# Kernel tuning notes

Hardware: AMD Instinct MI355X
Metric: run time of the kernel (lower is better)

## Reference

```python
import jax, jax.numpy as jnp
import numpy as np
import math

DMODEL, DK, H, DFF = 1024, 64, 16, 4096
B, T = 2, 2048
EPS = 1e-5


def setup_inputs() -> dict:
    key = jax.random.key(0)
    ks = jax.random.split(key, 12)
    s = 0.02
    x = jax.random.normal(ks[0], (B, T, DMODEL), dtype=jnp.float32)
    # causal mask, broadcastable [1,1,T,T]; 0 -> masked (like masked_fill(mask==0, -inf))
    attention_mask = jnp.tril(jnp.ones((T, T), dtype=jnp.int32))[None, None]
    Wq = jax.random.normal(ks[1], (DMODEL, DK * H), dtype=jnp.float32) * s
    bq = jnp.zeros((DK * H,), jnp.float32)
    Wk = jax.random.normal(ks[2], (DMODEL, DK * H), dtype=jnp.float32) * s
    bk = jnp.zeros((DK * H,), jnp.float32)
    Wv = jax.random.normal(ks[3], (DMODEL, DMODEL), dtype=jnp.float32) * s
    bv = jnp.zeros((DMODEL,), jnp.float32)
    W1 = jax.random.normal(ks[4], (DMODEL, DFF), dtype=jnp.float32) * s
    b1 = jnp.zeros((DFF,), jnp.float32)
    W2 = jax.random.normal(ks[5], (DFF, DMODEL), dtype=jnp.float32) * s
    b2 = jnp.zeros((DMODEL,), jnp.float32)
    g1 = jnp.ones((DMODEL,), jnp.float32)
    be1 = jnp.zeros((DMODEL,), jnp.float32)
    g2 = jnp.ones((DMODEL,), jnp.float32)
    be2 = jnp.zeros((DMODEL,), jnp.float32)
    return dict(x=x, attention_mask=attention_mask, Wq=Wq, bq=bq, Wk=Wk, bk=bk,
                Wv=Wv, bv=bv, W1=W1, b1=b1, W2=W2, b2=b2,
                g1=g1, be1=be1, g2=g2, be2=be2)


def _layernorm(x, g, b):
    mu = jnp.mean(x, axis=-1, keepdims=True)
    var = jnp.mean(jnp.square(x - mu), axis=-1, keepdims=True)
    return (x - mu) * jax.lax.rsqrt(var + EPS) * g + b


def _split_heads(t, h):  # [B,T,h*d] -> [B,h,T,d]
    Bn, Tn, D = t.shape
    return t.reshape(Bn, Tn, h, D // h).transpose(0, 2, 1, 3)


def reference(x, attention_mask, Wq, bq, Wk, bk, Wv, bv, W1, b1, W2, b2, g1, be1, g2, be2):
    # multi-head self-attention (hand-rolled, matching torch module)
    q = _split_heads(x @ Wq + bq, H)                    # [B,h,T,dk]
    k = _split_heads(x @ Wk + bk, H)                    # [B,h,T,dk]
    v = _split_heads(x @ Wv + bv, H)                    # [B,h,T,dv]
    scores = jnp.einsum('bhqd,bhkd->bhqk', q, k) / math.sqrt(DK)
    scores = jnp.where(attention_mask == 0, -jnp.inf, scores)
    probs = jax.nn.softmax(scores, axis=-1)
    attn = jnp.einsum('bhqk,bhkd->bhqd', probs, v)      # [B,h,T,dv]
    attn = attn.transpose(0, 2, 1, 3).reshape(B, T, DMODEL)
    # double residual (dropout = identity in eval): x + dropout(attn) + attn
    x1 = _layernorm(x + 2.0 * attn, g1, be1)
    ff = jax.nn.relu(x1 @ W1 + b1) @ W2 + b2
    out = _layernorm(x1 + 2.0 * ff, g2, be2)
    return out
```

## Files before the change

kernel.cpp:

```cpp
#include <hip/hip_runtime.h>

#define DMODEL 1024
#define DKH 64
#define NH 16
#define DFF 4096
#define BB 2
#define TT 2048
#define ROWS (BB*TT)
#define QKVN (3*DMODEL)

typedef unsigned short ushort_t;
typedef __attribute__((ext_vector_type(8))) short s8v;
typedef __attribute__((ext_vector_type(4))) float f4v;
typedef __attribute__((ext_vector_type(4))) unsigned short us4v;

typedef const void __attribute__((address_space(1)))* GPTR;
typedef void __attribute__((address_space(3)))* SPTR;

__device__ __forceinline__ float bf2f(ushort_t u) {
  return __uint_as_float(((unsigned int)u) << 16);
}
__device__ __forceinline__ ushort_t f2bf(float f) {
  unsigned int u = __float_as_uint(f);
  u += 0x7fffu + ((u >> 16) & 1u);
  return (ushort_t)(u >> 16);
}
__device__ __forceinline__ void gload16(const void* g, void* l) {
  __builtin_amdgcn_global_load_lds((GPTR)g, (SPTR)l, 16, 0, 0);
}

__global__ __launch_bounds__(256) void cvt_f32_bf16(const float* __restrict__ in,
                                                    ushort_t* __restrict__ out, int n4) {
  int i = blockIdx.x * 256 + threadIdx.x;
  if (i >= n4) return;
  float4 v = ((const float4*)in)[i];
  us4v o;
  o.x = f2bf(v.x); o.y = f2bf(v.y); o.z = f2bf(v.z); o.w = f2bf(v.w);
  ((us4v*)out)[i] = o;
}

__global__ __launch_bounds__(256) void transpose_cvt(const float* __restrict__ in,
                                                     ushort_t* __restrict__ out, int R, int C) {
  __shared__ float tile[32][33];
  int bx = blockIdx.x * 32, by = blockIdx.y * 32;
  int tx = threadIdx.x, ty = threadIdx.y;
#pragma unroll
  for (int i = 0; i < 32; i += 8)
    tile[ty + i][tx] = in[(size_t)(by + ty + i) * C + bx + tx];
  __syncthreads();
#pragma unroll
  for (int i = 0; i < 32; i += 8)
    out[(size_t)(bx + ty + i) * R + by + tx] = f2bf(tile[tx][ty + i]);
}

__global__ void concat_bias(const float* __restrict__ a, const float* __restrict__ b,
                            const float* __restrict__ c, float* __restrict__ o) {
  int i = blockIdx.x * 256 + threadIdx.x;
  if (i < 1024) { o[i] = a[i]; o[1024 + i] = b[i]; o[2048 + i] = c[i]; }
}

__global__ __launch_bounds__(256) void vtrans(const ushort_t* __restrict__ QKV,
                                              ushort_t* __restrict__ VT) {
  __shared__ ushort_t tile[32][66];
  const int t0 = blockIdx.x * 32;
  const int bh = blockIdx.y;
  const int b = bh >> 4, h = bh & 15;
  const int tx = threadIdx.x, ty = threadIdx.y;
  const ushort_t* src = QKV + ((size_t)b * TT + t0) * QKVN + 2 * DMODEL + h * 64;
#pragma unroll
  for (int i = 0; i < 4; ++i) {
    int r = ty + i * 8;
    *(unsigned int*)&tile[r][tx * 2] = *(const unsigned int*)(src + (size_t)r * QKVN + tx * 2);
  }
  __syncthreads();
  unsigned int* dst = (unsigned int*)(VT + (size_t)bh * 64 * TT);
#pragma unroll
  for (int i = 0; i < 4; ++i) {
    int d = ty + i * 8 + (tx >> 4) * 32;
    int p = tx & 15;
    unsigned int lo = tile[2 * p][d], hi = tile[2 * p + 1][d];
    dst[(size_t)d * (TT / 2) + (t0 >> 1) + p] = lo | (hi << 16);
  }
}

template<int MODE>
__global__ __launch_bounds__(256) void gemm128(const ushort_t* __restrict__ A,
                                               const ushort_t* __restrict__ BT,
                                               const float* __restrict__ bias,
                                               ushort_t* __restrict__ C,
                                               int M, int N, int Kstride, int Kloop,
                                               int nbx, int tiles_per_k) {
  __shared__ __align__(16) ushort_t As[2][128 * 64];
  __shared__ __align__(16) ushort_t Bs[2][128 * 64];
  const int nwg = gridDim.x;
  const int wg = blockIdx.x;
  const int cpx = nwg >> 3;
  const int swz = (wg & 7) * cpx + (wg >> 3);
  const int ks = swz / tiles_per_k;
  const int tile = swz % tiles_per_k;
  const int bx = tile % nbx, by = tile / nbx;
  const int m0 = by * 128, n0 = bx * 128;
  const size_t kbase = (size_t)ks * Kloop;
  const int tid = threadIdx.x;
  const int w = tid >> 6, l = tid & 63, lr = l & 15, lg = l >> 4;
  const int wm = w >> 1, wn = w & 1;

  const int sr = tid >> 3;
  const int scol = (((tid & 7) ^ (sr & 7)) << 3);

  auto stageA = [&](int kt, int buf) {
#pragma unroll
    for (int s = 0; s < 4; ++s)
      gload16(A + (size_t)(m0 + s * 32 + sr) * Kstride + kbase + kt * 64 + scol,
              (char*)&As[buf][0] + s * 4096 + tid * 16);
  };
  auto stageB = [&](int kt, int buf) {
#pragma unroll
    for (int s = 0; s < 4; ++s)
      gload16(BT + (size_t)(n0 + s * 32 + sr) * Kstride + kbase + kt * 64 + scol,
              (char*)&Bs[buf][0] + s * 4096 + tid * 16);
  };

  const int rsw = (lr & 7) << 4;
  auto ldA = [&](int buf, int m, int kk) -> s8v {
    return *(const s8v*)((const char*)&As[buf][0] +
                         (wm * 64 + m * 16 + lr) * 128 + ((kk * 64 + lg * 16) ^ rsw));
  };
  auto ldB = [&](int buf, int n, int kk) -> s8v {
    return *(const s8v*)((const char*)&Bs[buf][0] +
                         (wn * 64 + n * 16 + lr) * 128 + ((kk * 64 + lg * 16) ^ rsw));
  };

  f4v acc[4][4] = {};
  const int NT = Kloop >> 6;

  stageA(0, 0); stageB(0, 0);
  asm volatile("s_waitcnt vmcnt(0)" ::: "memory");
  __builtin_amdgcn_sched_barrier(0);
  __builtin_amdgcn_s_barrier();

  for (int t = 0; t < NT; ++t) {
    const int cb = t & 1, nb = cb ^ 1;
    if (t + 1 < NT) { stageA(t + 1, nb); stageB(t + 1, nb); }
    s8v af[2][4], bfr[2][4];
#pragma unroll
    for (int m = 0; m < 4; ++m) { af[0][m] = ldA(cb, m, 0); af[1][m] = ldA(cb, m, 1); }
#pragma unroll
    for (int n = 0; n < 4; ++n) { bfr[0][n] = ldB(cb, n, 0); bfr[1][n] = ldB(cb, n, 1); }
    __builtin_amdgcn_s_setprio(1);
#pragma unroll
    for (int m = 0; m < 4; ++m)
#pragma unroll
      for (int n = 0; n < 4; ++n) {
        acc[m][n] = __builtin_amdgcn_mfma_f32_16x16x32_bf16(af[0][m], bfr[0][n], acc[m][n], 0, 0, 0);
        acc[m][n] = __builtin_amdgcn_mfma_f32_16x16x32_bf16(af[1][m], bfr[1][n], acc[m][n], 0, 0, 0);
      }
    __builtin_amdgcn_s_setprio(0);
    if (t + 1 < NT) asm volatile("s_waitcnt vmcnt(0)" ::: "memory");
    __builtin_amdgcn_sched_barrier(0);
    __builtin_amdgcn_s_barrier();
  }

  ushort_t* Cp = (MODE == 2) ? (C + (size_t)ks * M * N) : C;
#pragma unroll
  for (int n = 0; n < 4; ++n) {
    int col = n0 + wn * 64 + n * 16 + lr;
    float bv = (MODE == 2) ? 0.f : bias[col];
#pragma unroll
    for (int m = 0; m < 4; ++m) {
      int row = m0 + wm * 64 + m * 16 + lg * 4;
#pragma unroll
      for (int j = 0; j < 4; ++j) {
        float v = acc[m][n][j] + bv;
        if (MODE == 1) v = fmaxf(v, 0.f);
        Cp[(size_t)(row + j) * N + col] = f2bf(v);
      }
    }
  }
}

__global__ __launch_bounds__(256) void attn_kernel(const ushort_t* __restrict__ QKV,
                                                   const ushort_t* __restrict__ VT,
                                                   ushort_t* __restrict__ O) {
  const int bh = blockIdx.x;
  const int qt = 31 - (int)blockIdx.y;
  const int b = bh >> 4, h = bh & 15;
  const int nkt = qt + 1;
  const int tid = threadIdx.x;
  const int w = tid >> 6, l = tid & 63;
  const int lr = l & 15, lg = l >> 4;

  __shared__ __align__(16) ushort_t Ksh[2][64 * 64];
  __shared__ __align__(16) ushort_t Vsh[64 * 64];
  __shared__ __align__(16) ushort_t Psh[4][16 * 72];

  const size_t RS = QKVN;
  const ushort_t* Qb = QKV + (size_t)b * TT * RS + h * 64;
  const ushort_t* Kb = Qb + DMODEL;
  const ushort_t* Vb = VT + (size_t)bh * 64 * TT;

  s8v qf[2];
  {
    const ushort_t* qr = Qb + (size_t)(qt * 64 + w * 16 + lr) * RS + lg * 8;
    qf[0] = *(const s8v*)qr;
    qf[1] = *(const s8v*)(qr + 32);
  }
  f4v acc[4] = {};
  float lrow = 0.f;

  const int sr8 = l >> 3, sc = l & 7;

  auto stageK = [&](int kt, int buf) {
#pragma unroll
    for (int s = 0; s < 2; ++s) {
      int r = s * 32 + w * 8 + sr8;
      gload16(Kb + (size_t)(kt * 64 + r) * RS + ((sc ^ (r & 7)) << 3),
              (char*)&Ksh[buf][0] + (s * 32 + w * 8) * 128 + l * 16);
    }
  };
  auto stageV = [&](int kt) {
#pragma unroll
    for (int s = 0; s < 2; ++s) {
      int r = s * 32 + w * 8 + sr8;
      gload16(Vb + (size_t)r * TT + kt * 64 + ((sc ^ (r & 7)) << 3),
              (char*)&Vsh[0] + (s * 32 + w * 8) * 128 + l * 16);
    }
  };

  stageK(0, 0);
  for (int kt = 0; kt < nkt; ++kt) {
    const int cb = kt & 1;
    const bool last = (kt + 1 >= nkt);
    stageV(kt);
    if (!last) {
      stageK(kt + 1, cb ^ 1);
      asm volatile("s_waitcnt vmcnt(4)" ::: "memory");
    } else {
      asm volatile("s_waitcnt vmcnt(2)" ::: "memory");
    }
    __builtin_amdgcn_sched_barrier(0);
    __builtin_amdgcn_s_barrier();

    float ps = 0.f;
#pragma unroll
    for (int c = 0; c < 4; ++c) {
      f4v a = {};
      __builtin_amdgcn_s_setprio(1);
#pragma unroll
      for (int kk = 0; kk < 2; ++kk) {
        int rr = c * 16 + lr;
        int byte_ = (rr * 128 + kk * 64 + lg * 16) ^ ((rr & 7) << 4);
        s8v kf = *(const s8v*)((const char*)&Ksh[cb][0] + byte_);
        a = __builtin_amdgcn_mfma_f32_16x16x32_bf16(kf, qf[kk], a, 0, 0, 0);
      }
      __builtin_amdgcn_s_setprio(0);
      float e[4];
#pragma unroll
      for (int j = 0; j < 4; ++j) {
        e[j] = __expf(a[j] * 0.125f);
        if (last && (c * 16 + lg * 4 + j > w * 16 + lr)) e[j] = 0.f;
        ps += e[j];
      }
      unsigned int pk0, pk1;
      asm("v_cvt_pk_bf16_f32 %0, %1, %2" : "=v"(pk0) : "v"(e[0]), "v"(e[1]));
      asm("v_cvt_pk_bf16_f32 %0, %1, %2" : "=v"(pk1) : "v"(e[2]), "v"(e[3]));
      *(uint2*)((char*)&Psh[w][0] + lr * 144 + (c * 16 + lg * 4) * 2) = make_uint2(pk0, pk1);
    }
    s8v pa[2];
    pa[0] = *(const s8v*)((const char*)&Psh[w][0] + lr * 144 + lg * 16);
    pa[1] = *(const s8v*)((const char*)&Psh[w][0] + lr * 144 + 64 + lg * 16);

    if (!last) {
      asm volatile("s_waitcnt vmcnt(2)" ::: "memory");
    } else {
      asm volatile("s_waitcnt vmcnt(0)" ::: "memory");
    }
    __builtin_amdgcn_sched_barrier(0);
    __builtin_amdgcn_s_barrier();

    __builtin_amdgcn_s_setprio(1);
#pragma unroll
    for (int ks = 0; ks < 2; ++ks)
#pragma unroll
      for (int d = 0; d < 4; ++d) {
        int row = d * 16 + lr;
        int byte_ = (row * 128 + ks * 64 + lg * 16) ^ ((row & 7) << 4);
        s8v vf = *(const s8v*)((const char*)&Vsh[0] + byte_);
        acc[d] = __builtin_amdgcn_mfma_f32_16x16x32_bf16(pa[ks], vf, acc[d], 0, 0, 0);
      }
    __builtin_amdgcn_s_setprio(0);
    ps += __shfl_xor(ps, 16);
    ps += __shfl_xor(ps, 32);
    lrow += ps;
    __builtin_amdgcn_s_barrier();
  }

  float inv = 1.f / lrow;
  ushort_t* orow = O + ((size_t)b * TT + qt * 64 + w * 16) * DMODEL + h * 64;
#pragma unroll
  for (int j = 0; j < 4; ++j) {
    float invj = __shfl(inv, lg * 4 + j);
#pragma unroll
    for (int d = 0; d < 4; ++d)
      orow[(size_t)(lg * 4 + j) * DMODEL + d * 16 + lr] = f2bf(acc[d][j] * invj);
  }
}

__global__ __launch_bounds__(256) void ln_kernel(const float* __restrict__ aptr,
                                                 const ushort_t* __restrict__ bptr,
                                                 const float* __restrict__ g,
                                                 const float* __restrict__ be,
                                                 ushort_t* __restrict__ yptr) {
  const int row = blockIdx.x;
  const int t = threadIdx.x;
  const int w = t >> 6, l = t & 63;
  const size_t base = (size_t)row * DMODEL + t * 4;
  float v[4];
  us4v bb = *(const us4v*)(bptr + base);
  float4 xa = *(const float4*)(aptr + base);
  v[0] = xa.x + 2.f * bf2f(bb.x);
  v[1] = xa.y + 2.f * bf2f(bb.y);
  v[2] = xa.z + 2.f * bf2f(bb.z);
  v[3] = xa.w + 2.f * bf2f(bb.w);
  float s = v[0] + v[1] + v[2] + v[3];
  float s2 = v[0] * v[0] + v[1] * v[1] + v[2] * v[2] + v[3] * v[3];
#pragma unroll
  for (int off = 1; off <= 32; off <<= 1) {
    s += __shfl_xor(s, off);
    s2 += __shfl_xor(s2, off);
  }
  __shared__ float red[2][4];
  if (l == 0) { red[0][w] = s; red[1][w] = s2; }
  __syncthreads();
  s = red[0][0] + red[0][1] + red[0][2] + red[0][3];
  s2 = red[1][0] + red[1][1] + red[1][2] + red[1][3];
  const float mu = s * (1.f / 1024.f);
  const float var = s2 * (1.f / 1024.f) - mu * mu;
  const float rstd = rsqrtf(var + 1e-5f);
  float4 g4 = *(const float4*)(g + t * 4);
  float4 be4 = *(const float4*)(be + t * 4);
  us4v o;
  o.x = f2bf((v[0] - mu) * rstd * g4.x + be4.x);
  o.y = f2bf((v[1] - mu) * rstd * g4.y + be4.y);
  o.z = f2bf((v[2] - mu) * rstd * g4.z + be4.z);
  o.w = f2bf((v[3] - mu) * rstd * g4.w + be4.w);
  *(us4v*)(yptr + base) = o;
}

__global__ __launch_bounds__(256) void ln2_kernel(const ushort_t* __restrict__ x1,
                                                  const ushort_t* __restrict__ part,
                                                  const float* __restrict__ b2,
                                                  const float* __restrict__ g,
                                                  const float* __restrict__ be,
                                                  float* __restrict__ y) {
  const int row = blockIdx.x;
  const int t = threadIdx.x;
  const int w = t >> 6, l = t & 63;
  const size_t base = (size_t)row * DMODEL + t * 4;
  us4v xa = *(const us4v*)(x1 + base);
  float f[4] = {0.f, 0.f, 0.f, 0.f};
#pragma unroll
  for (int ks = 0; ks < 4; ++ks) {
    us4v p = *(const us4v*)(part + (size_t)ks * ROWS * DMODEL + base);
    f[0] += bf2f(p.x); f[1] += bf2f(p.y); f[2] += bf2f(p.z); f[3] += bf2f(p.w);
  }
  float4 b2v = *(const float4*)(b2 + t * 4);
  float v[4];
  v[0] = bf2f(xa.x) + 2.f * (f[0] + b2v.x);
  v[1] = bf2f(xa.y) + 2.f * (f[1] + b2v.y);
  v[2] = bf2f(xa.z) + 2.f * (f[2] + b2v.z);
  v[3] = bf2f(xa.w) + 2.f * (f[3] + b2v.w);
  float s = v[0] + v[1] + v[2] + v[3];
  float s2 = v[0] * v[0] + v[1] * v[1] + v[2] * v[2] + v[3] * v[3];
#pragma unroll
  for (int off = 1; off <= 32; off <<= 1) {
    s += __shfl_xor(s, off);
    s2 += __shfl_xor(s2, off);
  }
  __shared__ float red[2][4];
  if (l == 0) { red[0][w] = s; red[1][w] = s2; }
  __syncthreads();
  s = red[0][0] + red[0][1] + red[0][2] + red[0][3];
  s2 = red[1][0] + red[1][1] + red[1][2] + red[1][3];
  const float mu = s * (1.f / 1024.f);
  const float var = s2 * (1.f / 1024.f) - mu * mu;
  const float rstd = rsqrtf(var + 1e-5f);
  float4 g4 = *(const float4*)(g + t * 4);
  float4 be4 = *(const float4*)(be + t * 4);
  float4 o;
  o.x = (v[0] - mu) * rstd * g4.x + be4.x;
  o.y = (v[1] - mu) * rstd * g4.y + be4.y;
  o.z = (v[2] - mu) * rstd * g4.z + be4.z;
  o.w = (v[3] - mu) * rstd * g4.w + be4.w;
  *(float4*)(y + base) = o;
}

extern "C" void kernel_launch(void* const* d_in, const int* in_sizes, int n_in,
                              void* d_out, int out_size, void* d_ws, size_t ws_size,
                              hipStream_t stream) {
  const float* x   = (const float*)d_in[0];
  const float* Wq  = (const float*)d_in[2];
  const float* bq  = (const float*)d_in[3];
  const float* Wk  = (const float*)d_in[4];
  const float* bk  = (const float*)d_in[5];
  const float* Wv  = (const float*)d_in[6];
  const float* bv  = (const float*)d_in[7];
  const float* W1  = (const float*)d_in[8];
  const float* b1  = (const float*)d_in[9];
  const float* W2  = (const float*)d_in[10];
  const float* b2  = (const float*)d_in[11];
  const float* g1  = (const float*)d_in[12];
  const float* be1 = (const float*)d_in[13];
  const float* g2  = (const float*)d_in[14];
  const float* be2 = (const float*)d_in[15];
  float* out = (float*)d_out;

  char* ws = (char*)d_ws;
  size_t off = 0;
  auto alloc = [&](size_t bytes) {
    char* p = ws + off;
    off += (bytes + 255) & ~(size_t)255;
    return p;
  };
  ushort_t* xb    = (ushort_t*)alloc((size_t)ROWS * DMODEL * 2);
  ushort_t* WqkvT = (ushort_t*)alloc((size_t)QKVN * DMODEL * 2);
  ushort_t* W1T   = (ushort_t*)alloc((size_t)DFF * DMODEL * 2);
  ushort_t* W2T   = (ushort_t*)alloc((size_t)DMODEL * DFF * 2);
  ushort_t* QKV   = (ushort_t*)alloc((size_t)ROWS * QKVN * 2);
  ushort_t* VTb   = (ushort_t*)alloc((size_t)BB * NH * 64 * TT * 2);
  ushort_t* attnb = (ushort_t*)alloc((size_t)ROWS * DMODEL * 2);
  ushort_t* x1b   = (ushort_t*)alloc((size_t)ROWS * DMODEL * 2);
  ushort_t* H1b   = (ushort_t*)alloc((size_t)ROWS * DFF * 2);
  float* qkvb     = (float*)alloc(QKVN * 4);
  ushort_t* part  = QKV;
  (void)ws_size; (void)in_sizes; (void)n_in; (void)out_size;

  dim3 b256(256);
  dim3 tb(32, 8);
  cvt_f32_bf16<<<ROWS * DMODEL / 4 / 256, b256, 0, stream>>>(x, xb, ROWS * DMODEL / 4);
  transpose_cvt<<<dim3(32, 32), tb, 0, stream>>>(Wq, WqkvT, DMODEL, DMODEL);
  transpose_cvt<<<dim3(32, 32), tb, 0, stream>>>(Wk, WqkvT + DMODEL * DMODEL, DMODEL, DMODEL);
  transpose_cvt<<<dim3(32, 32), tb, 0, stream>>>(Wv, WqkvT + 2 * DMODEL * DMODEL, DMODEL, DMODEL);
  transpose_cvt<<<dim3(DFF / 32, DMODEL / 32), tb, 0, stream>>>(W1, W1T, DMODEL, DFF);
  transpose_cvt<<<dim3(DMODEL / 32, DFF / 32), tb, 0, stream>>>(W2, W2T, DFF, DMODEL);
  concat_bias<<<4, b256, 0, stream>>>(bq, bk, bv, qkvb);

  gemm128<0><<<dim3(768), b256, 0, stream>>>(xb, WqkvT, qkvb, QKV,
                                             ROWS, QKVN, DMODEL, DMODEL,
                                             QKVN / 128, 768);
  vtrans<<<dim3(TT / 32, BB * NH), tb, 0, stream>>>(QKV, VTb);
  attn_kernel<<<dim3(BB * NH, 32), b256, 0, stream>>>(QKV, VTb, attnb);
  ln_kernel<<<ROWS, b256, 0, stream>>>(x, attnb, g1, be1, x1b);
  gemm128<1><<<dim3(1024), b256, 0, stream>>>(x1b, W1T, b1, H1b,
                                              ROWS, DFF, DMODEL, DMODEL,
                                              DFF / 128, 1024);
  gemm128<2><<<dim3(1024), b256, 0, stream>>>(H1b, W2T, b2, part,
                                              ROWS, DMODEL, DFF, DFF / 4,
                                              DMODEL / 128, 256);
  ln2_kernel<<<ROWS, b256, 0, stream>>>(x1b, part, b2, g2, be2, out);
}
```

Baseline: 220.3 us.

## Merge weight transposes, fold softmax scale into Q, reorder attention tiles, halve W2 split-K

Merges the five weight-transpose launches into two z-indexed kernels. Folds the 1/sqrt(dk)·log2(e) scale into the QKV GEMM epilogue (new MODE 3) so attention can use exp2f directly. Interleaves the attention query-tile order in a snake pattern to balance causal work across blocks. Reduces the W2 GEMM split-K from 4 to 2 partitions, which means fewer blocks and fewer partial sums for the final layernorm to read. Storing Q pre-scaled in bf16 changes rounding slightly.

New measurement: 224.1 us. About the same (+1.7%).

```diff
diff --git a/kernel.cpp b/kernel.cpp
--- a/kernel.cpp
+++ b/kernel.cpp
@@ -8,6 +8,7 @@
 #define TT 2048
 #define ROWS (BB*TT)
 #define QKVN (3*DMODEL)
+#define QSCALE 0.18033688011112042f
 
 typedef unsigned short ushort_t;
 typedef __attribute__((ext_vector_type(8))) short s8v;
@@ -39,10 +40,36 @@
   ((us4v*)out)[i] = o;
 }
 
-__global__ __launch_bounds__(256) void transpose_cvt(const float* __restrict__ in,
-                                                     ushort_t* __restrict__ out, int R, int C) {
+__global__ __launch_bounds__(256) void trans_qkv(const float* __restrict__ w0,
+                                                 const float* __restrict__ w1,
+                                                 const float* __restrict__ w2,
+                                                 ushort_t* __restrict__ out) {
   __shared__ float tile[32][33];
+  const float* in = (blockIdx.z == 0) ? w0 : (blockIdx.z == 1) ? w1 : w2;
+  ushort_t* dst = out + (size_t)blockIdx.z * DMODEL * DMODEL;
   int bx = blockIdx.x * 32, by = blockIdx.y * 32;
+  int tx = threadIdx.x, ty = threadIdx.y;
+#pragma unroll
+  for (int i = 0; i < 32; i += 8)
+    tile[ty + i][tx] = in[(size_t)(by + ty + i) * DMODEL + bx + tx];
+  __syncthreads();
+#pragma unroll
+  for (int i = 0; i < 32; i += 8)
+    dst[(size_t)(bx + ty + i) * DMODEL + by + tx] = f2bf(tile[tx][ty + i]);
+}
+
+__global__ __launch_bounds__(256) void trans_ffn(const float* __restrict__ W1,
+                                                 const float* __restrict__ W2,
+                                                 ushort_t* __restrict__ W1T,
+                                                 ushort_t* __restrict__ W2T) {
+  __shared__ float tile[32][33];
+  const int z = blockIdx.z;
+  const float* in = z ? W2 : W1;
+  ushort_t* dst = z ? W2T : W1T;
+  const int R = z ? DFF : DMODEL;
+  const int C = z ? DMODEL : DFF;
+  int bx = (z ? blockIdx.y : blockIdx.x) * 32;
+  int by = (z ? blockIdx.x : blockIdx.y) * 32;
   int tx = threadIdx.x, ty = threadIdx.y;
 #pragma unroll
   for (int i = 0; i < 32; i += 8)
@@ -50,7 +77,7 @@
   __syncthreads();
 #pragma unroll
   for (int i = 0; i < 32; i += 8)
-    out[(size_t)(bx + ty + i) * R + by + tx] = f2bf(tile[tx][ty + i]);
+    dst[(size_t)(bx + ty + i) * R + by + tx] = f2bf(tile[tx][ty + i]);
 }
 
 __global__ void concat_bias(const float* __restrict__ a, const float* __restrict__ b,
@@ -106,7 +133,7 @@
   const int wm = w >> 1, wn = w & 1;
 
   const int sr = tid >> 3;
-  const int scol = (((tid & 7) ^ (sr & 7)) << 3);
+  const int scol = (((tid & 7) ^ ((tid >> 3) & 7)) << 3);
 
   auto stageA = [&](int kt, int buf) {
 #pragma unroll
@@ -166,6 +193,7 @@
   for (int n = 0; n < 4; ++n) {
     int col = n0 + wn * 64 + n * 16 + lr;
     float bv = (MODE == 2) ? 0.f : bias[col];
+    float sc = (MODE == 3 && col < DMODEL) ? QSCALE : 1.f;
 #pragma unroll
     for (int m = 0; m < 4; ++m) {
       int row = m0 + wm * 64 + m * 16 + lg * 4;
@@ -173,6 +201,7 @@
       for (int j = 0; j < 4; ++j) {
         float v = acc[m][n][j] + bv;
         if (MODE == 1) v = fmaxf(v, 0.f);
+        if (MODE == 3) v *= sc;
         Cp[(size_t)(row + j) * N + col] = f2bf(v);
       }
     }
@@ -183,7 +212,9 @@
                                                    const ushort_t* __restrict__ VT,
                                                    ushort_t* __restrict__ O) {
   const int bh = blockIdx.x;
-  const int qt = 31 - (int)blockIdx.y;
+  const int byy = blockIdx.y;
+  const int kk_ = byy >> 3, rr_ = byy & 7;
+  const int qt = (kk_ & 1) ? (8 * kk_ + 7 - rr_) : (8 * kk_ + rr_);
   const int b = bh >> 4, h = bh & 15;
   const int nkt = qt + 1;
   const int tid = threadIdx.x;
@@ -257,7 +288,7 @@
       float e[4];
 #pragma unroll
       for (int j = 0; j < 4; ++j) {
-        e[j] = __expf(a[j] * 0.125f);
+        e[j] = exp2f(a[j]);
         if (last && (c * 16 + lg * 4 + j > w * 16 + lr)) e[j] = 0.f;
         ps += e[j];
       }
@@ -360,7 +391,7 @@
   us4v xa = *(const us4v*)(x1 + base);
   float f[4] = {0.f, 0.f, 0.f, 0.f};
 #pragma unroll
-  for (int ks = 0; ks < 4; ++ks) {
+  for (int ks = 0; ks < 2; ++ks) {
     us4v p = *(const us4v*)(part + (size_t)ks * ROWS * DMODEL + base);
     f[0] += bf2f(p.x); f[1] += bf2f(p.y); f[2] += bf2f(p.z); f[3] += bf2f(p.w);
   }
@@ -438,14 +469,11 @@
   dim3 b256(256);
   dim3 tb(32, 8);
   cvt_f32_bf16<<<ROWS * DMODEL / 4 / 256, b256, 0, stream>>>(x, xb, ROWS * DMODEL / 4);
-  transpose_cvt<<<dim3(32, 32), tb, 0, stream>>>(Wq, WqkvT, DMODEL, DMODEL);
-  transpose_cvt<<<dim3(32, 32), tb, 0, stream>>>(Wk, WqkvT + DMODEL * DMODEL, DMODEL, DMODEL);
-  transpose_cvt<<<dim3(32, 32), tb, 0, stream>>>(Wv, WqkvT + 2 * DMODEL * DMODEL, DMODEL, DMODEL);
-  transpose_cvt<<<dim3(DFF / 32, DMODEL / 32), tb, 0, stream>>>(W1, W1T, DMODEL, DFF);
-  transpose_cvt<<<dim3(DMODEL / 32, DFF / 32), tb, 0, stream>>>(W2, W2T, DFF, DMODEL);
+  trans_qkv<<<dim3(32, 32, 3), tb, 0, stream>>>(Wq, Wk, Wv, WqkvT);
+  trans_ffn<<<dim3(DFF / 32, DMODEL / 32, 2), tb, 0, stream>>>(W1, W2, W1T, W2T);
   concat_bias<<<4, b256, 0, stream>>>(bq, bk, bv, qkvb);
 
-  gemm128<0><<<dim3(768), b256, 0, stream>>>(xb, WqkvT, qkvb, QKV,
+  gemm128<3><<<dim3(768), b256, 0, stream>>>(xb, WqkvT, qkvb, QKV,
                                              ROWS, QKVN, DMODEL, DMODEL,
                                              QKVN / 128, 768);
   vtrans<<<dim3(TT / 32, BB * NH), tb, 0, stream>>>(QKV, VTb);
@@ -454,8 +482,8 @@
   gemm128<1><<<dim3(1024), b256, 0, stream>>>(x1b, W1T, b1, H1b,
                                               ROWS, DFF, DMODEL, DMODEL,
                                               DFF / 128, 1024);
-  gemm128<2><<<dim3(1024), b256, 0, stream>>>(H1b, W2T, b2, part,
-                                              ROWS, DMODEL, DFF, DFF / 4,
-                                              DMODEL / 128, 256);
+  gemm128<2><<<dim3(512), b256, 0, stream>>>(H1b, W2T, b2, part,
+                                             ROWS, DMODEL, DFF, DFF / 2,
+                                             DMODEL / 128, 256);
   ln2_kernel<<<ROWS, b256, 0, stream>>>(x1b, part, b2, g2, be2, out);
 }
```
